# Optimization experiments

Hardware: AMD Instinct MI355X
Metric: run time of the kernel (lower is better)

Reference implementation:

```python
import jax, jax.numpy as jnp
import numpy as np

N_NODES = 100000
N_EDGES = 3200000
D_IN, D_HID, D_OUT = 512, 256, 64


def setup_inputs() -> dict:
    key = jax.random.key(0)
    ks = jax.random.split(key, 8)
    x = jax.random.normal(ks[0], (N_NODES, D_IN), dtype=jnp.float32)
    row = jax.random.randint(ks[1], (N_EDGES,), 0, N_NODES, dtype=jnp.int64)
    col = jax.random.randint(ks[2], (N_EDGES,), 0, N_NODES, dtype=jnp.int64)
    edge_weight = jax.random.uniform(ks[3], (N_EDGES,), dtype=jnp.float32)
    w1 = jax.random.normal(ks[4], (D_IN, D_HID), dtype=jnp.float32) * (1.0 / np.sqrt(D_HID))
    b1 = jax.random.normal(ks[5], (D_HID,), dtype=jnp.float32) * (1.0 / np.sqrt(D_HID))
    w2 = jax.random.normal(ks[6], (D_HID, D_OUT), dtype=jnp.float32) * (1.0 / np.sqrt(D_OUT))
    b2 = jax.random.normal(ks[7], (D_OUT,), dtype=jnp.float32) * (1.0 / np.sqrt(D_OUT))
    return {"x": x, "row": row, "col": col, "edge_weight": edge_weight,
            "w1": w1, "b1": b1, "w2": w2, "b2": b2}


def _gc_layer(h, row, col, edge_weight, w, b, n_nodes):
    # support = h @ w ; out = spmm(adj, support) + b
    support = h @ w                                   # [N, d_out]
    msgs = edge_weight[:, None] * support[col]        # gather source rows
    agg = jax.ops.segment_sum(msgs, row, num_segments=n_nodes)
    return agg + b


def reference(x, row, col, edge_weight, w1, b1, w2, b2):
    n = x.shape[0]
    h = jax.nn.relu(_gc_layer(x, row, col, edge_weight, w1, b1, n))
    # dropout p=0.0 -> identity
    h = _gc_layer(h, row, col, edge_weight, w2, b2, n)
    return jax.nn.log_softmax(h, axis=1)
```

## Files before the change

kernel.cpp:

```cpp
#include <hip/hip_runtime.h>
#include <hip/hip_bf16.h>

#define N_NODES 100000
#define N_EDGES 3200000
#define D_IN 512
#define D_HID 256
#define D_OUT 64
#define M_PAD 100096

#define NB 782
#define EPB 8192
#define NBLK_BIN ((N_EDGES + EPB - 1) / EPB)

typedef __attribute__((ext_vector_type(8))) short bf16x8;
typedef __attribute__((ext_vector_type(4))) float f32x4;

__device__ __forceinline__ unsigned short f2bf(float f) {
    __hip_bfloat16 h = __float2bfloat16(f);
    return *reinterpret_cast<unsigned short*>(&h);
}
__device__ __forceinline__ float bf_lo(unsigned int v) { return __uint_as_float(v << 16); }
__device__ __forceinline__ float bf_hi(unsigned int v) { return __uint_as_float(v & 0xffff0000u); }


__global__ void cast_x_kernel(const float* __restrict__ x, __hip_bfloat16* __restrict__ xb) {
    long long i8 = ((long long)blockIdx.x * 256 + threadIdx.x) * 8;
    const long long total = (long long)M_PAD * D_IN;
    if (i8 >= total) return;
    int r = (int)(i8 / D_IN);
    ushort4 o0, o1;
    if (r < N_NODES) {
        float4 a = *reinterpret_cast<const float4*>(&x[i8]);
        float4 b = *reinterpret_cast<const float4*>(&x[i8 + 4]);
        o0 = {f2bf(a.x), f2bf(a.y), f2bf(a.z), f2bf(a.w)};
        o1 = {f2bf(b.x), f2bf(b.y), f2bf(b.z), f2bf(b.w)};
    } else {
        o0 = {0, 0, 0, 0};
        o1 = {0, 0, 0, 0};
    }
    *reinterpret_cast<ushort4*>(&xb[i8]) = o0;
    *reinterpret_cast<ushort4*>(&xb[i8 + 4]) = o1;
}

__global__ void cast_w1t_kernel(const float* __restrict__ w1, __hip_bfloat16* __restrict__ w1t) {
    int i = blockIdx.x * 256 + threadIdx.x;
    if (i >= D_IN * D_HID) return;
    int k = i / D_HID, n = i % D_HID;
    w1t[n * D_IN + k] = __float2bfloat16(w1[i]);
}

__global__ void cast_w2t_kernel(const float* __restrict__ w2, __hip_bfloat16* __restrict__ w2t) {
    int i = blockIdx.x * 256 + threadIdx.x;
    if (i >= D_HID * D_OUT) return;
    int k = i / D_OUT, n = i % D_OUT;
    w2t[n * D_HID + k] = __float2bfloat16(w2[i]);
}


__global__ __launch_bounds__(256) void hist_bucket_kernel(const int* __restrict__ row,
                                                          int* __restrict__ gcnt) {
    __shared__ int cnt[NB];
    for (int i = threadIdx.x; i < NB; i += 256) cnt[i] = 0;
    __syncthreads();
    int base = blockIdx.x * EPB;
    for (int i = threadIdx.x; i < EPB; i += 256) {
        int e = base + i;
        if (e < N_EDGES) atomicAdd(&cnt[row[e] >> 7], 1);
    }
    __syncthreads();
    for (int i = threadIdx.x; i < NB; i += 256) {
        int c = cnt[i];
        if (c) atomicAdd(&gcnt[i], c);
    }
}

__global__ void scan_nb_kernel(const int* __restrict__ gcnt, int* __restrict__ boff,
                               int* __restrict__ gcur, int* __restrict__ offsets) {
    __shared__ int smem[1024];
    int t = threadIdx.x;
    int v = (t < NB) ? gcnt[t] : 0;
    smem[t] = v;
    __syncthreads();
    for (int off = 1; off < 1024; off <<= 1) {
        int u = (t >= off) ? smem[t - off] : 0;
        __syncthreads();
        smem[t] += u;
        __syncthreads();
    }
    int excl = smem[t] - v;
    if (t < NB) { boff[t] = excl; gcur[t] = excl; }
    if (t == 1023) boff[NB] = smem[1023];
    if (t == 0) offsets[N_NODES] = N_EDGES;
}

__global__ __launch_bounds__(256) void bin_kernel(const int* __restrict__ row,
                                                  const int* __restrict__ col,
                                                  const float* __restrict__ ew,
                                                  int* __restrict__ gcur,
                                                  int2* __restrict__ bucketed) {
    __shared__ int cnt[NB];
    __shared__ int cur[NB];
    for (int i = threadIdx.x; i < NB; i += 256) cnt[i] = 0;
    __syncthreads();
    int base = blockIdx.x * EPB;
    for (int i = threadIdx.x; i < EPB; i += 256) {
        int e = base + i;
        if (e < N_EDGES) atomicAdd(&cnt[row[e] >> 7], 1);
    }
    __syncthreads();
    for (int i = threadIdx.x; i < NB; i += 256) {
        int c = cnt[i];
        cur[i] = c ? atomicAdd(&gcur[i], c) : 0;
    }
    __syncthreads();
    for (int i = threadIdx.x; i < EPB; i += 256) {
        int e = base + i;
        if (e < N_EDGES) {
            int r = row[e];
            int b = r >> 7;
            int pos = atomicAdd(&cur[b], 1);
            bucketed[pos] = make_int2((col[e] << 7) | (r & 127), __float_as_int(ew[e]));
        }
    }
}

__global__ __launch_bounds__(256) void csr_kernel(const int2* __restrict__ bucketed,
                                                  const int* __restrict__ boff,
                                                  int* __restrict__ offsets,
                                                  int2* __restrict__ edges) {
    __shared__ int rcnt[128];
    __shared__ int sc[128];
    __shared__ int rcur[128];
    int b = blockIdx.x;
    int t = threadIdx.x;
    int s = boff[b], e2 = boff[b + 1];
    if (t < 128) rcnt[t] = 0;
    __syncthreads();
    for (int i = s + t; i < e2; i += 256) atomicAdd(&rcnt[bucketed[i].x & 127], 1);
    __syncthreads();
    if (t < 128) sc[t] = rcnt[t];
    __syncthreads();
    for (int off = 1; off < 128; off <<= 1) {
        int u = 0;
        if (t < 128 && t >= off) u = sc[t - off];
        __syncthreads();
        if (t < 128) sc[t] += u;
        __syncthreads();
    }
    if (t < 128) {
        int excl = sc[t] - rcnt[t];
        rcur[t] = excl;
        int rglob = b * 128 + t;
        if (rglob < N_NODES) offsets[rglob] = s + excl;
    }
    __syncthreads();
    for (int i = s + t; i < e2; i += 256) {
        int2 p = bucketed[i];
        int r = p.x & 127;
        int pos = atomicAdd(&rcur[r], 1);
        edges[s + pos] = make_int2(p.x >> 7, p.y);
    }
}


template <int BN, int WROWS, int WCOLS, int MT, int NT, bool OUT_BF16>
__global__ __launch_bounds__(256) void gemm_bf16_kernel(
    const __hip_bfloat16* __restrict__ A, const __hip_bfloat16* __restrict__ Bt,
    void* __restrict__ Cv, int K, int Mvalid, int Nld) {
    constexpr int BM = 128;
    constexpr int BK = 32;
    constexpr int LDT = BK + 8;
    __shared__ __align__(16) __hip_bfloat16 As[BM][LDT];
    __shared__ __align__(16) __hip_bfloat16 Bs[BN][LDT];

    const int tid = threadIdx.x;
    const int m0 = blockIdx.x * BM;
    const int n0 = blockIdx.y * BN;
    const int w = tid >> 6, lane = tid & 63;
    const int wr = w % WROWS, wc = w / WROWS;
    const int mbase = wr * MT * 16, nbase = wc * NT * 16;
    const int quad = lane >> 4, l16 = lane & 15;

    f32x4 acc[MT][NT] = {};

    constexpr int ACH = (BM * BK) / (256 * 8);
    constexpr int BCH = (BN * BK) / (256 * 8);

    for (int k0 = 0; k0 < K; k0 += BK) {
#pragma unroll
        for (int c = 0; c < ACH; ++c) {
            int idx = (tid + c * 256) * 8;
            int r = idx / BK, kk = idx % BK;
            *reinterpret_cast<uint4*>(&As[r][kk]) =
                *reinterpret_cast<const uint4*>(&A[(size_t)(m0 + r) * K + k0 + kk]);
        }
#pragma unroll
        for (int c = 0; c < BCH; ++c) {
            int idx = (tid + c * 256) * 8;
            int r = idx / BK, kk = idx % BK;
            *reinterpret_cast<uint4*>(&Bs[r][kk]) =
                *reinterpret_cast<const uint4*>(&Bt[(size_t)(n0 + r) * K + k0 + kk]);
        }
        __syncthreads();

        bf16x8 af[MT], bfr[NT];
#pragma unroll
        for (int mt = 0; mt < MT; ++mt)
            af[mt] = *reinterpret_cast<bf16x8*>(&As[mbase + mt * 16 + l16][quad * 8]);
#pragma unroll
        for (int nt = 0; nt < NT; ++nt)
            bfr[nt] = *reinterpret_cast<bf16x8*>(&Bs[nbase + nt * 16 + l16][quad * 8]);
#pragma unroll
        for (int mt = 0; mt < MT; ++mt)
#pragma unroll
            for (int nt = 0; nt < NT; ++nt)
                acc[mt][nt] = __builtin_amdgcn_mfma_f32_16x16x32_bf16(af[mt], bfr[nt],
                                                                      acc[mt][nt], 0, 0, 0);
        __syncthreads();
    }

#pragma unroll
    for (int mt = 0; mt < MT; ++mt)
#pragma unroll
        for (int nt = 0; nt < NT; ++nt)
#pragma unroll
            for (int r = 0; r < 4; ++r) {
                int rowi = m0 + mbase + mt * 16 + quad * 4 + r;
                int coli = n0 + nbase + nt * 16 + l16;
                if (rowi < Mvalid) {
                    if constexpr (OUT_BF16) {
                        ((__hip_bfloat16*)Cv)[(size_t)rowi * Nld + coli] =
                            __float2bfloat16(acc[mt][nt][r]);
                    } else {
                        ((float*)Cv)[(size_t)rowi * Nld + coli] = acc[mt][nt][r];
                    }
                }
            }
}


__global__ __launch_bounds__(256) void agg1_kernel(
    const unsigned short* __restrict__ sup, const int* __restrict__ offsets,
    const int2* __restrict__ edges, const float* __restrict__ b1,
    __hip_bfloat16* __restrict__ hb) {
    int n = blockIdx.x * 4 + (threadIdx.x >> 6);
    int lane = threadIdx.x & 63;
    const int coloff = lane * 4;
    if (n >= M_PAD) return;
    if (n >= N_NODES) {
        *reinterpret_cast<ushort4*>(&hb[(size_t)n * D_HID + coloff]) = ushort4{0, 0, 0, 0};
        return;
    }
    int s = offsets[n], e2 = offsets[n + 1];
    float a0 = 0.f, a1 = 0.f, a2 = 0.f, a3 = 0.f;
    int e = s;
    for (; e + 4 <= e2; e += 4) {
        int2 m0 = edges[e], m1 = edges[e + 1], m2 = edges[e + 2], m3 = edges[e + 3];
        uint2 v0 = *reinterpret_cast<const uint2*>(sup + (size_t)m0.x * D_HID + coloff);
        uint2 v1 = *reinterpret_cast<const uint2*>(sup + (size_t)m1.x * D_HID + coloff);
        uint2 v2 = *reinterpret_cast<const uint2*>(sup + (size_t)m2.x * D_HID + coloff);
        uint2 v3 = *reinterpret_cast<const uint2*>(sup + (size_t)m3.x * D_HID + coloff);
        float w0 = __int_as_float(m0.y), w1 = __int_as_float(m1.y);
        float w2 = __int_as_float(m2.y), w3 = __int_as_float(m3.y);
        a0 += w0 * bf_lo(v0.x); a1 += w0 * bf_hi(v0.x); a2 += w0 * bf_lo(v0.y); a3 += w0 * bf_hi(v0.y);
        a0 += w1 * bf_lo(v1.x); a1 += w1 * bf_hi(v1.x); a2 += w1 * bf_lo(v1.y); a3 += w1 * bf_hi(v1.y);
        a0 += w2 * bf_lo(v2.x); a1 += w2 * bf_hi(v2.x); a2 += w2 * bf_lo(v2.y); a3 += w2 * bf_hi(v2.y);
        a0 += w3 * bf_lo(v3.x); a1 += w3 * bf_hi(v3.x); a2 += w3 * bf_lo(v3.y); a3 += w3 * bf_hi(v3.y);
    }
    for (; e < e2; ++e) {
        int2 m = edges[e];
        uint2 v = *reinterpret_cast<const uint2*>(sup + (size_t)m.x * D_HID + coloff);
        float wv = __int_as_float(m.y);
        a0 += wv * bf_lo(v.x); a1 += wv * bf_hi(v.x); a2 += wv * bf_lo(v.y); a3 += wv * bf_hi(v.y);
    }
    float4 bb = reinterpret_cast<const float4*>(b1)[lane];
    ushort4 o;
    o.x = f2bf(fmaxf(a0 + bb.x, 0.f));
    o.y = f2bf(fmaxf(a1 + bb.y, 0.f));
    o.z = f2bf(fmaxf(a2 + bb.z, 0.f));
    o.w = f2bf(fmaxf(a3 + bb.w, 0.f));
    *reinterpret_cast<ushort4*>(&hb[(size_t)n * D_HID + coloff]) = o;
}

__global__ __launch_bounds__(256) void agg2_softmax_kernel(
    const unsigned short* __restrict__ sup2, const int* __restrict__ offsets,
    const int2* __restrict__ edges, const float* __restrict__ b2, float* __restrict__ out) {
    int n = blockIdx.x * 4 + (threadIdx.x >> 6);
    int j = threadIdx.x & 63;
    if (n >= N_NODES) return;
    int s = offsets[n], e2 = offsets[n + 1];
    float acc = 0.f;
    int e = s;
    for (; e + 4 <= e2; e += 4) {
        int2 m0 = edges[e], m1 = edges[e + 1], m2 = edges[e + 2], m3 = edges[e + 3];
        float v0 = __uint_as_float((unsigned)sup2[(size_t)m0.x * D_OUT + j] << 16);
        float v1 = __uint_as_float((unsigned)sup2[(size_t)m1.x * D_OUT + j] << 16);
        float v2 = __uint_as_float((unsigned)sup2[(size_t)m2.x * D_OUT + j] << 16);
        float v3 = __uint_as_float((unsigned)sup2[(size_t)m3.x * D_OUT + j] << 16);
        acc += __int_as_float(m0.y) * v0;
        acc += __int_as_float(m1.y) * v1;
        acc += __int_as_float(m2.y) * v2;
        acc += __int_as_float(m3.y) * v3;
    }
    for (; e < e2; ++e) {
        int2 m = edges[e];
        acc += __int_as_float(m.y) * __uint_as_float((unsigned)sup2[(size_t)m.x * D_OUT + j] << 16);
    }
    acc += b2[j];
    float m = acc;
#pragma unroll
    for (int o = 32; o > 0; o >>= 1) m = fmaxf(m, __shfl_xor(m, o, 64));
    float ex = __expf(acc - m);
    float ssum = ex;
#pragma unroll
    for (int o = 32; o > 0; o >>= 1) ssum += __shfl_xor(ssum, o, 64);
    out[(size_t)n * D_OUT + j] = acc - m - __logf(ssum);
}


extern "C" void kernel_launch(void* const* d_in, const int* in_sizes, int n_in,
                              void* d_out, int out_size, void* d_ws, size_t ws_size,
                              hipStream_t stream) {
    const float* x  = (const float*)d_in[0];
    const int* row  = (const int*)d_in[1];
    const int* col  = (const int*)d_in[2];
    const float* ew = (const float*)d_in[3];
    const float* w1 = (const float*)d_in[4];
    const float* b1 = (const float*)d_in[5];
    const float* w2 = (const float*)d_in[6];
    const float* b2 = (const float*)d_in[7];
    float* out = (float*)d_out;

    char* ws = (char*)d_ws;
    size_t off = 0;
    auto alloc = [&](size_t bytes) -> void* {
        void* p = ws + off;
        off = (off + bytes + 255) & ~(size_t)255;
        return p;
    };

    __hip_bfloat16* xb   = (__hip_bfloat16*)alloc((size_t)M_PAD * D_IN * 2);
    __hip_bfloat16* w1t  = (__hip_bfloat16*)alloc((size_t)D_HID * D_IN * 2);
    __hip_bfloat16* w2t  = (__hip_bfloat16*)alloc((size_t)D_OUT * D_HID * 2);
    __hip_bfloat16* sup1 = (__hip_bfloat16*)alloc((size_t)N_NODES * D_HID * 2);
    __hip_bfloat16* hb   = (__hip_bfloat16*)alloc((size_t)M_PAD * D_HID * 2);
    int* offsets         = (int*)alloc((size_t)(N_NODES + 1) * 4);
    int* gcnt            = (int*)alloc((size_t)NB * 4);
    int* boff            = (int*)alloc((size_t)(NB + 1) * 4);
    int* gcur            = (int*)alloc((size_t)NB * 4);
    int2* edges          = (int2*)alloc((size_t)N_EDGES * 8);
    int2* bucketed       = (int2*)xb;
    unsigned short* sup2 = (unsigned short*)xb;

    hipMemsetAsync(gcnt, 0, (size_t)NB * 4, stream);
    hist_bucket_kernel<<<NBLK_BIN, 256, 0, stream>>>(row, gcnt);
    scan_nb_kernel<<<1, 1024, 0, stream>>>(gcnt, boff, gcur, offsets);
    bin_kernel<<<NBLK_BIN, 256, 0, stream>>>(row, col, ew, gcur, bucketed);
    csr_kernel<<<NB, 256, 0, stream>>>(bucketed, boff, offsets, edges);

    cast_x_kernel<<<(M_PAD * D_IN / 8 + 255) / 256, 256, 0, stream>>>(x, xb);
    cast_w1t_kernel<<<(D_IN * D_HID + 255) / 256, 256, 0, stream>>>(w1, w1t);
    cast_w2t_kernel<<<(D_HID * D_OUT + 255) / 256, 256, 0, stream>>>(w2, w2t);

    gemm_bf16_kernel<128, 2, 2, 4, 4, true><<<dim3(M_PAD / 128, D_HID / 128), 256, 0, stream>>>(
        xb, w1t, sup1, D_IN, N_NODES, D_HID);
    agg1_kernel<<<M_PAD / 4, 256, 0, stream>>>((const unsigned short*)sup1, offsets, edges, b1, hb);

    gemm_bf16_kernel<64, 4, 1, 2, 4, true><<<dim3(M_PAD / 128, 1), 256, 0, stream>>>(
        hb, w2t, (void*)sup2, D_HID, N_NODES, D_OUT);
    agg2_softmax_kernel<<<(N_NODES + 3) / 4, 256, 0, stream>>>(sup2, offsets, edges, b2, out);
}
```

Measured before the change: 846.8 us.

## Fuse x cast into GEMM1 and store layer-1 support as FP8

Removes the separate fp32-to-bf16 cast pass over x by converting to bf16 inside the first GEMM's A-tile load, with zero padding for out-of-range rows. The first GEMM now writes its support matrix as FP8 e4m3 instead of bf16, which halves the bytes gathered per edge in the layer-1 aggregation. That aggregation reads one 32-bit word (four FP8 values) per lane and unrolls the edge loop by 8. Buffers that used to alias the xb scratch now get their own allocations. FP8 support lowers precision in the main gather and may exceed the accuracy tolerance.

```diff
diff --git a/kernel.cpp b/kernel.cpp
--- a/kernel.cpp
+++ b/kernel.cpp
@@ -1,5 +1,6 @@
 #include <hip/hip_runtime.h>
 #include <hip/hip_bf16.h>
+#include <hip/hip_fp8.h>
 
 #define N_NODES 100000
 #define N_EDGES 3200000
@@ -19,28 +20,12 @@
     __hip_bfloat16 h = __float2bfloat16(f);
     return *reinterpret_cast<unsigned short*>(&h);
 }
-__device__ __forceinline__ float bf_lo(unsigned int v) { return __uint_as_float(v << 16); }
-__device__ __forceinline__ float bf_hi(unsigned int v) { return __uint_as_float(v & 0xffff0000u); }
-
-
-__global__ void cast_x_kernel(const float* __restrict__ x, __hip_bfloat16* __restrict__ xb) {
-    long long i8 = ((long long)blockIdx.x * 256 + threadIdx.x) * 8;
-    const long long total = (long long)M_PAD * D_IN;
-    if (i8 >= total) return;
-    int r = (int)(i8 / D_IN);
-    ushort4 o0, o1;
-    if (r < N_NODES) {
-        float4 a = *reinterpret_cast<const float4*>(&x[i8]);
-        float4 b = *reinterpret_cast<const float4*>(&x[i8 + 4]);
-        o0 = {f2bf(a.x), f2bf(a.y), f2bf(a.z), f2bf(a.w)};
-        o1 = {f2bf(b.x), f2bf(b.y), f2bf(b.z), f2bf(b.w)};
-    } else {
-        o0 = {0, 0, 0, 0};
-        o1 = {0, 0, 0, 0};
-    }
-    *reinterpret_cast<ushort4*>(&xb[i8]) = o0;
-    *reinterpret_cast<ushort4*>(&xb[i8 + 4]) = o1;
-}
+__device__ __forceinline__ float f8f(unsigned int byte) {
+    __hip_fp8_e4m3 t;
+    t.__x = (__hip_fp8_storage_t)byte;
+    return (float)t;
+}
+
 
 __global__ void cast_w1t_kernel(const float* __restrict__ w1, __hip_bfloat16* __restrict__ w1t) {
     int i = blockIdx.x * 256 + threadIdx.x;
@@ -163,9 +148,9 @@
 }
 
 
-template <int BN, int WROWS, int WCOLS, int MT, int NT, bool OUT_BF16>
+template <int BN, int WROWS, int WCOLS, int MT, int NT, bool A_F32, int OUT_MODE>
 __global__ __launch_bounds__(256) void gemm_bf16_kernel(
-    const __hip_bfloat16* __restrict__ A, const __hip_bfloat16* __restrict__ Bt,
+    const void* __restrict__ Av, const __hip_bfloat16* __restrict__ Bt,
     void* __restrict__ Cv, int K, int Mvalid, int Nld) {
     constexpr int BM = 128;
     constexpr int BK = 32;
@@ -191,8 +176,25 @@
         for (int c = 0; c < ACH; ++c) {
             int idx = (tid + c * 256) * 8;
             int r = idx / BK, kk = idx % BK;
-            *reinterpret_cast<uint4*>(&As[r][kk]) =
-                *reinterpret_cast<const uint4*>(&A[(size_t)(m0 + r) * K + k0 + kk]);
+            if constexpr (A_F32) {
+                int grow = m0 + r;
+                uint4 o;
+                if (grow < Mvalid) {
+                    const float* ap = (const float*)Av + (size_t)grow * K + k0 + kk;
+                    float4 f0 = *reinterpret_cast<const float4*>(ap);
+                    float4 f1 = *reinterpret_cast<const float4*>(ap + 4);
+                    o.x = (unsigned)f2bf(f0.x) | ((unsigned)f2bf(f0.y) << 16);
+                    o.y = (unsigned)f2bf(f0.z) | ((unsigned)f2bf(f0.w) << 16);
+                    o.z = (unsigned)f2bf(f1.x) | ((unsigned)f2bf(f1.y) << 16);
+                    o.w = (unsigned)f2bf(f1.z) | ((unsigned)f2bf(f1.w) << 16);
+                } else {
+                    o = uint4{0, 0, 0, 0};
+                }
+                *reinterpret_cast<uint4*>(&As[r][kk]) = o;
+            } else {
+                *reinterpret_cast<uint4*>(&As[r][kk]) = *reinterpret_cast<const uint4*>(
+                    (const __hip_bfloat16*)Av + (size_t)(m0 + r) * K + k0 + kk);
+            }
         }
 #pragma unroll
         for (int c = 0; c < BCH; ++c) {
@@ -228,11 +230,14 @@
                 int rowi = m0 + mbase + mt * 16 + quad * 4 + r;
                 int coli = n0 + nbase + nt * 16 + l16;
                 if (rowi < Mvalid) {
-                    if constexpr (OUT_BF16) {
+                    if constexpr (OUT_MODE == 0) {
+                        ((float*)Cv)[(size_t)rowi * Nld + coli] = acc[mt][nt][r];
+                    } else if constexpr (OUT_MODE == 1) {
                         ((__hip_bfloat16*)Cv)[(size_t)rowi * Nld + coli] =
                             __float2bfloat16(acc[mt][nt][r]);
                     } else {
-                        ((float*)Cv)[(size_t)rowi * Nld + coli] = acc[mt][nt][r];
+                        __hip_fp8_e4m3 q(acc[mt][nt][r]);
+                        ((unsigned char*)Cv)[(size_t)rowi * Nld + coli] = q.__x;
                     }
                 }
             }
@@ -240,38 +245,43 @@
 
 
 __global__ __launch_bounds__(256) void agg1_kernel(
-    const unsigned short* __restrict__ sup, const int* __restrict__ offsets,
-    const int2* __restrict__ edges, const float* __restrict__ b1,
-    __hip_bfloat16* __restrict__ hb) {
+    const unsigned int* __restrict__ sup,
+    const int* __restrict__ offsets, const int2* __restrict__ edges,
+    const float* __restrict__ b1, __hip_bfloat16* __restrict__ hb) {
     int n = blockIdx.x * 4 + (threadIdx.x >> 6);
     int lane = threadIdx.x & 63;
-    const int coloff = lane * 4;
     if (n >= M_PAD) return;
     if (n >= N_NODES) {
-        *reinterpret_cast<ushort4*>(&hb[(size_t)n * D_HID + coloff]) = ushort4{0, 0, 0, 0};
+        *reinterpret_cast<ushort4*>(&hb[(size_t)n * D_HID + lane * 4]) = ushort4{0, 0, 0, 0};
         return;
     }
     int s = offsets[n], e2 = offsets[n + 1];
     float a0 = 0.f, a1 = 0.f, a2 = 0.f, a3 = 0.f;
     int e = s;
-    for (; e + 4 <= e2; e += 4) {
-        int2 m0 = edges[e], m1 = edges[e + 1], m2 = edges[e + 2], m3 = edges[e + 3];
-        uint2 v0 = *reinterpret_cast<const uint2*>(sup + (size_t)m0.x * D_HID + coloff);
-        uint2 v1 = *reinterpret_cast<const uint2*>(sup + (size_t)m1.x * D_HID + coloff);
-        uint2 v2 = *reinterpret_cast<const uint2*>(sup + (size_t)m2.x * D_HID + coloff);
-        uint2 v3 = *reinterpret_cast<const uint2*>(sup + (size_t)m3.x * D_HID + coloff);
-        float w0 = __int_as_float(m0.y), w1 = __int_as_float(m1.y);
-        float w2 = __int_as_float(m2.y), w3 = __int_as_float(m3.y);
-        a0 += w0 * bf_lo(v0.x); a1 += w0 * bf_hi(v0.x); a2 += w0 * bf_lo(v0.y); a3 += w0 * bf_hi(v0.y);
-        a0 += w1 * bf_lo(v1.x); a1 += w1 * bf_hi(v1.x); a2 += w1 * bf_lo(v1.y); a3 += w1 * bf_hi(v1.y);
-        a0 += w2 * bf_lo(v2.x); a1 += w2 * bf_hi(v2.x); a2 += w2 * bf_lo(v2.y); a3 += w2 * bf_hi(v2.y);
-        a0 += w3 * bf_lo(v3.x); a1 += w3 * bf_hi(v3.x); a2 += w3 * bf_lo(v3.y); a3 += w3 * bf_hi(v3.y);
+    for (; e + 8 <= e2; e += 8) {
+        int2 m[8];
+        unsigned int v[8];
+#pragma unroll
+        for (int i = 0; i < 8; ++i) m[i] = edges[e + i];
+#pragma unroll
+        for (int i = 0; i < 8; ++i) v[i] = sup[(size_t)m[i].x * 64 + lane];
+#pragma unroll
+        for (int i = 0; i < 8; ++i) {
+            float wv = __int_as_float(m[i].y);
+            a0 += wv * f8f(v[i] & 0xff);
+            a1 += wv * f8f((v[i] >> 8) & 0xff);
+            a2 += wv * f8f((v[i] >> 16) & 0xff);
+            a3 += wv * f8f(v[i] >> 24);
+        }
     }
     for (; e < e2; ++e) {
         int2 m = edges[e];
-        uint2 v = *reinterpret_cast<const uint2*>(sup + (size_t)m.x * D_HID + coloff);
+        unsigned int v = sup[(size_t)m.x * 64 + lane];
         float wv = __int_as_float(m.y);
-        a0 += wv * bf_lo(v.x); a1 += wv * bf_hi(v.x); a2 += wv * bf_lo(v.y); a3 += wv * bf_hi(v.y);
+        a0 += wv * f8f(v & 0xff);
+        a1 += wv * f8f((v >> 8) & 0xff);
+        a2 += wv * f8f((v >> 16) & 0xff);
+        a3 += wv * f8f(v >> 24);
     }
     float4 bb = reinterpret_cast<const float4*>(b1)[lane];
     ushort4 o;
@@ -279,7 +289,7 @@
     o.y = f2bf(fmaxf(a1 + bb.y, 0.f));
     o.z = f2bf(fmaxf(a2 + bb.z, 0.f));
     o.w = f2bf(fmaxf(a3 + bb.w, 0.f));
-    *reinterpret_cast<ushort4*>(&hb[(size_t)n * D_HID + coloff]) = o;
+    *reinterpret_cast<ushort4*>(&hb[(size_t)n * D_HID + lane * 4]) = o;
 }
 
 __global__ __launch_bounds__(256) void agg2_softmax_kernel(
@@ -339,18 +349,17 @@
         return p;
     };
 
-    __hip_bfloat16* xb   = (__hip_bfloat16*)alloc((size_t)M_PAD * D_IN * 2);
     __hip_bfloat16* w1t  = (__hip_bfloat16*)alloc((size_t)D_HID * D_IN * 2);
     __hip_bfloat16* w2t  = (__hip_bfloat16*)alloc((size_t)D_OUT * D_HID * 2);
-    __hip_bfloat16* sup1 = (__hip_bfloat16*)alloc((size_t)N_NODES * D_HID * 2);
+    unsigned char* sup1  = (unsigned char*)alloc((size_t)N_NODES * D_HID);
     __hip_bfloat16* hb   = (__hip_bfloat16*)alloc((size_t)M_PAD * D_HID * 2);
+    unsigned short* sup2 = (unsigned short*)alloc((size_t)N_NODES * D_OUT * 2);
     int* offsets         = (int*)alloc((size_t)(N_NODES + 1) * 4);
     int* gcnt            = (int*)alloc((size_t)NB * 4);
     int* boff            = (int*)alloc((size_t)(NB + 1) * 4);
     int* gcur            = (int*)alloc((size_t)NB * 4);
     int2* edges          = (int2*)alloc((size_t)N_EDGES * 8);
-    int2* bucketed       = (int2*)xb;
-    unsigned short* sup2 = (unsigned short*)xb;
+    int2* bucketed       = (int2*)alloc((size_t)N_EDGES * 8);
 
     hipMemsetAsync(gcnt, 0, (size_t)NB * 4, stream);
     hist_bucket_kernel<<<NBLK_BIN, 256, 0, stream>>>(row, gcnt);
@@ -358,15 +367,14 @@
     bin_kernel<<<NBLK_BIN, 256, 0, stream>>>(row, col, ew, gcur, bucketed);
     csr_kernel<<<NB, 256, 0, stream>>>(bucketed, boff, offsets, edges);
 
-    cast_x_kernel<<<(M_PAD * D_IN / 8 + 255) / 256, 256, 0, stream>>>(x, xb);
     cast_w1t_kernel<<<(D_IN * D_HID + 255) / 256, 256, 0, stream>>>(w1, w1t);
     cast_w2t_kernel<<<(D_HID * D_OUT + 255) / 256, 256, 0, stream>>>(w2, w2t);
 
-    gemm_bf16_kernel<128, 2, 2, 4, 4, true><<<dim3(M_PAD / 128, D_HID / 128), 256, 0, stream>>>(
-        xb, w1t, sup1, D_IN, N_NODES, D_HID);
-    agg1_kernel<<<M_PAD / 4, 256, 0, stream>>>((const unsigned short*)sup1, offsets, edges, b1, hb);
-
-    gemm_bf16_kernel<64, 4, 1, 2, 4, true><<<dim3(M_PAD / 128, 1), 256, 0, stream>>>(
-        hb, w2t, (void*)sup2, D_HID, N_NODES, D_OUT);
+    gemm_bf16_kernel<128, 2, 2, 4, 4, true, 2><<<dim3(M_PAD / 128, D_HID / 128), 256, 0, stream>>>(
+        x, w1t, sup1, D_IN, N_NODES, D_HID);
+    agg1_kernel<<<M_PAD / 4, 256, 0, stream>>>((const unsigned int*)sup1, offsets, edges, b1, hb);
+
+    gemm_bf16_kernel<64, 4, 1, 2, 4, false, 1><<<dim3(M_PAD / 128, 1), 256, 0, stream>>>(
+        hb, w2t, sup2, D_HID, N_NODES, D_OUT);
     agg2_softmax_kernel<<<(N_NODES + 3) / 4, 256, 0, stream>>>(sup2, offsets, edges, b2, out);
 }
```

Measured after the change: 770.3 us. -9.0%, faster.
